# Optimization experiments

Measured on AMD Instinct MI355X. Metric: run time of the kernel, lower is better.

The kernel has to match this reference:

```python
import jax, jax.numpy as jnp
import numpy as np

DIM = 96
NUM_HEADS = 3
WIN = (4, 4, 4)
SHIFT = (2, 2, 2)
MLP_HID = 4 * DIM
EPS = 1e-5


def layer_norm(x, w, b):
    mu = jnp.mean(x, axis=-1, keepdims=True)
    var = jnp.var(x, axis=-1, keepdims=True)
    return (x - mu) * jax.lax.rsqrt(var + EPS) * w + b


def window_partition(x, ws):
    b, d, h, w, c = x.shape
    x = x.reshape(b, d // ws[0], ws[0], h // ws[1], ws[1], w // ws[2], ws[2], c)
    x = jnp.transpose(x, (0, 1, 3, 5, 2, 4, 6, 7))
    return x.reshape(-1, ws[0] * ws[1] * ws[2], c)


def window_reverse(windows, ws, dims):
    b, d, h, w = dims
    x = windows.reshape(b, d // ws[0], h // ws[1], w // ws[2], ws[0], ws[1], ws[2], -1)
    x = jnp.transpose(x, (0, 1, 4, 2, 5, 3, 6, 7))
    return x.reshape(b, d, h, w, -1)


def setup_inputs() -> dict:
    key = jax.random.key(0)
    ks = jax.random.split(key, 14)
    C, H3 = DIM, MLP_HID
    s = lambda k, shp, sc: (jax.random.normal(k, shp, dtype=jnp.float32) * sc)
    return {
        "x": jax.random.normal(ks[0], (2, 32, 64, 64, C), dtype=jnp.float32),
        "ln1_w": jnp.ones((C,), jnp.float32),
        "ln1_b": jnp.zeros((C,), jnp.float32),
        "qkv_w": s(ks[1], (3 * C, C), 0.02),
        "qkv_b": jnp.zeros((3 * C,), jnp.float32),
        "proj_w": s(ks[2], (C, C), 0.02),
        "proj_b": jnp.zeros((C,), jnp.float32),
        "ln2_w": jnp.ones((C,), jnp.float32),
        "ln2_b": jnp.zeros((C,), jnp.float32),
        "fc1_w": s(ks[3], (H3, C), 0.02),
        "fc1_b": jnp.zeros((H3,), jnp.float32),
        "fc2_w": s(ks[4], (C, H3), 0.02),
        "fc2_b": jnp.zeros((C,), jnp.float32),
    }


def reference(x, ln1_w, ln1_b, qkv_w, qkv_b, proj_w, proj_b, ln2_w, ln2_b,
              fc1_w, fc1_b, fc2_w, fc2_b):
    B, D, H, W, C = x.shape
    nh = NUM_HEADS
    hd = C // nh
    scale = hd ** -0.5
    N = WIN[0] * WIN[1] * WIN[2]

    shortcut = x
    h = layer_norm(x, ln1_w, ln1_b)
    # cyclic shift
    h = jnp.roll(h, shift=(-SHIFT[0], -SHIFT[1], -SHIFT[2]), axis=(1, 2, 3))
    xw = window_partition(h, WIN)                     # [B*nW, N, C]
    Bw = xw.shape[0]

    # window attention (no mask / no relative bias in original forward)
    qkv = xw @ qkv_w.T + qkv_b                        # [Bw, N, 3C]
    qkv = qkv.reshape(Bw, N, 3, nh, hd).transpose(2, 0, 3, 1, 4)
    q, k, v = qkv[0], qkv[1], qkv[2]                  # [Bw, nh, N, hd]
    attn = jnp.einsum('bhnd,bhmd->bhnm', q * scale, k)
    attn = jax.nn.softmax(attn, axis=-1)
    out = jnp.einsum('bhnm,bhmd->bhnd', attn, v)
    out = out.transpose(0, 2, 1, 3).reshape(Bw, N, C)
    out = out @ proj_w.T + proj_b

    h = window_reverse(out, WIN, (B, D, H, W))
    h = jnp.roll(h, shift=SHIFT, axis=(1, 2, 3))
    x = shortcut + h

    # MLP with exact GELU (torch nn.GELU default)
    m = layer_norm(x, ln2_w, ln2_b)
    m = jax.nn.gelu(m @ fc1_w.T + fc1_b, approximate=False)
    m = m @ fc2_w.T + fc2_b
    return x + m
```

## Files before the change

kernel.cpp:

```cpp
#include <hip/hip_runtime.h>
#include <hip/hip_bf16.h>
#include <math.h>

typedef __hip_bfloat16 bf16;
using short8 = __attribute__((ext_vector_type(8))) short;
using f32x4  = __attribute__((ext_vector_type(4))) float;

__device__ __forceinline__ bf16 f2b(float v){ return __float2bfloat16(v); }
__device__ __forceinline__ float gelu_exact(float v){ return 0.5f * v * (1.f + erff(v * 0.70710678118654752f)); }

__global__ __launch_bounds__(256)
void prep_weights(const float* __restrict__ qkv_w, const float* __restrict__ proj_w,
                  const float* __restrict__ fc1_w, const float* __restrict__ fc2_w,
                  bf16* __restrict__ ws)
{
    const int t = blockIdx.x * 256 + threadIdx.x;
    const int f = t >> 6;
    const int lane = t & 63;
    const float* W; int KT, fr; bf16* dst;
    if (f < 54)       { W = qkv_w;  KT = 3;  fr = f;       dst = ws; }
    else if (f < 72)  { W = proj_w; KT = 3;  fr = f - 54;  dst = ws + 54*512; }
    else if (f < 144) { W = fc1_w;  KT = 3;  fr = f - 72;  dst = ws + 72*512; }
    else              { W = fc2_w;  KT = 12; fr = f - 144; dst = ws + 144*512; }
    const int nt = fr / KT, kt = fr % KT;
    const int Kin = KT * 32;
    const float* src = W + (nt*16 + (lane & 15))*Kin + kt*32 + 8*(lane >> 4);
    bf16* d = dst + fr*512 + lane*8;
    #pragma unroll
    for (int i = 0; i < 8; i++) d[i] = f2b(src[i]);
}

__global__ __launch_bounds__(256, 3)
void swin_fused(const float* __restrict__ x,
                const float* __restrict__ ln1_w, const float* __restrict__ ln1_b,
                const float* __restrict__ qkv_b, const float* __restrict__ proj_b,
                const float* __restrict__ ln2_w, const float* __restrict__ ln2_b,
                const float* __restrict__ fc1_b, const float* __restrict__ fc2_b,
                const bf16* __restrict__ wsf,
                float* __restrict__ out)
{
    __shared__ int tok_off[64];
    __shared__ __align__(16) char pool[50688];
    bf16 (*ln_s)[104] = (bf16(*)[104])(pool + 0);
    bf16 (*q_s)[40]   = (bf16(*)[40])(pool + 13312);
    bf16 (*k_s)[40]   = (bf16(*)[40])(pool + 18432);
    bf16 (*vt_s)[72]  = (bf16(*)[72])(pool + 23552);
    bf16 (*p_s)[72]   = (bf16(*)[72])(pool + 28160);
    bf16 (*ao_s)[104] = (bf16(*)[104])(pool + 37376);
    bf16 (*ln2s)[104] = ao_s;
    bf16 (*hid)[392]  = (bf16(*)[392])(pool + 0);

    const int tid = threadIdx.x;
    const int win = blockIdx.x;
    const int b  = win >> 11;
    const int wd = (win >> 8) & 7;
    const int wh = (win >> 4) & 15;
    const int ww = win & 15;

    if (tid < 64) {
        const int n  = tid;
        const int df = (wd*4 + (n >> 4)       + 2) & 31;
        const int hf = (wh*4 + ((n >> 2) & 3) + 2) & 63;
        const int wf = (ww*4 + (n & 3)        + 2) & 63;
        tok_off[n] = (((b*32 + df)*64 + hf)*64 + wf) * 96;
    }
    __syncthreads();

    {
        const int lane = tid & 63;
        const int n    = (tid >> 6)*16 + (lane >> 2);
        const int sub  = lane & 3;
        const float4* xr4 = (const float4*)(x + tok_off[n] + sub*24);
        float4 va[6];
        float s = 0.f, ss = 0.f;
        #pragma unroll
        for (int i = 0; i < 6; i++) {
            va[i] = xr4[i];
            s  += va[i].x + va[i].y + va[i].z + va[i].w;
            ss += va[i].x*va[i].x + va[i].y*va[i].y + va[i].z*va[i].z + va[i].w*va[i].w;
        }
        s += __shfl_xor(s, 1); ss += __shfl_xor(ss, 1);
        s += __shfl_xor(s, 2); ss += __shfl_xor(ss, 2);
        const float mean = s * (1.f/96.f);
        const float var  = ss * (1.f/96.f) - mean*mean;
        const float inv  = rsqrtf(var + 1e-5f);
        #pragma unroll
        for (int i = 0; i < 6; i++) {
            const float vv[4] = {va[i].x, va[i].y, va[i].z, va[i].w};
            #pragma unroll
            for (int j2 = 0; j2 < 4; j2++) {
                const int c = sub*24 + i*4 + j2;
                ln_s[n][c] = f2b((vv[j2] - mean) * inv * ln1_w[c] + ln1_b[c]);
            }
        }
    }
    __syncthreads();

    const int w    = tid >> 6;
    const int lane = tid & 63;
    const int lc   = lane & 15;
    const int lr   = lane >> 4;
    const int m0   = w * 16;
    const int tokr = m0 + lr*4;
    const float scale = 0.17677669529663688f;

    short8 lnA[3];
    #pragma unroll
    for (int kt = 0; kt < 3; kt++)
        lnA[kt] = *(const short8*)&ln_s[m0 + lc][kt*32 + 8*lr];

    for (int h = 0; h < 3; h++) {
        #pragma unroll
        for (int nt2 = 0; nt2 < 2; nt2++) {
            const int dd = nt2*16 + lc;
            {
                f32x4 acc = {0.f,0.f,0.f,0.f};
                #pragma unroll
                for (int kt = 0; kt < 3; kt++)
                    acc = __builtin_amdgcn_mfma_f32_16x16x32_bf16(
                        lnA[kt], *(const short8*)(wsf + ((2*h+nt2)*3+kt)*512 + lane*8), acc, 0,0,0);
                const float bias = qkv_b[h*32 + dd];
                #pragma unroll
                for (int r = 0; r < 4; r++)
                    q_s[tokr + r][dd] = f2b((acc[r] + bias) * scale);
            }
            {
                f32x4 acc = {0.f,0.f,0.f,0.f};
                #pragma unroll
                for (int kt = 0; kt < 3; kt++)
                    acc = __builtin_amdgcn_mfma_f32_16x16x32_bf16(
                        lnA[kt], *(const short8*)(wsf + ((6+2*h+nt2)*3+kt)*512 + lane*8), acc, 0,0,0);
                const float bias = qkv_b[96 + h*32 + dd];
                #pragma unroll
                for (int r = 0; r < 4; r++)
                    k_s[tokr + r][dd] = f2b(acc[r] + bias);
            }
            {
                f32x4 acc = {0.f,0.f,0.f,0.f};
                #pragma unroll
                for (int kt = 0; kt < 3; kt++)
                    acc = __builtin_amdgcn_mfma_f32_16x16x32_bf16(
                        *(const short8*)(wsf + ((12+2*h+nt2)*3+kt)*512 + lane*8), lnA[kt], acc, 0,0,0);
                #pragma unroll
                for (int r = 0; r < 4; r++) {
                    const int dl = nt2*16 + lr*4 + r;
                    vt_s[dl][m0 + lc] = f2b(acc[r] + qkv_b[192 + h*32 + dl]);
                }
            }
        }
        __syncthreads();

        {
            const short8 qf = *(const short8*)&q_s[m0 + lc][8*lr];
            f32x4 sacc[4];
            #pragma unroll
            for (int nt = 0; nt < 4; nt++) {
                f32x4 z = {0.f,0.f,0.f,0.f};
                sacc[nt] = __builtin_amdgcn_mfma_f32_16x16x32_bf16(
                    qf, *(const short8*)&k_s[nt*16 + lc][8*lr], z, 0,0,0);
            }
            #pragma unroll
            for (int r = 0; r < 4; r++) {
                float mx = fmaxf(fmaxf(sacc[0][r], sacc[1][r]), fmaxf(sacc[2][r], sacc[3][r]));
                mx = fmaxf(mx, __shfl_xor(mx, 1));
                mx = fmaxf(mx, __shfl_xor(mx, 2));
                mx = fmaxf(mx, __shfl_xor(mx, 4));
                mx = fmaxf(mx, __shfl_xor(mx, 8));
                float e[4], sum = 0.f;
                #pragma unroll
                for (int nt = 0; nt < 4; nt++) { e[nt] = __expf(sacc[nt][r] - mx); sum += e[nt]; }
                sum += __shfl_xor(sum, 1);
                sum += __shfl_xor(sum, 2);
                sum += __shfl_xor(sum, 4);
                sum += __shfl_xor(sum, 8);
                const float rs = 1.f / sum;
                #pragma unroll
                for (int nt = 0; nt < 4; nt++)
                    p_s[tokr + r][nt*16 + lc] = f2b(e[nt] * rs);
            }
        }

        {
            short8 pf[2];
            #pragma unroll
            for (int kt = 0; kt < 2; kt++)
                pf[kt] = *(const short8*)&p_s[m0 + lc][kt*32 + 8*lr];
            #pragma unroll
            for (int nt = 0; nt < 2; nt++) {
                f32x4 acc = {0.f,0.f,0.f,0.f};
                #pragma unroll
                for (int kt = 0; kt < 2; kt++)
                    acc = __builtin_amdgcn_mfma_f32_16x16x32_bf16(
                        pf[kt], *(const short8*)&vt_s[nt*16 + lc][kt*32 + 8*lr], acc, 0,0,0);
                #pragma unroll
                for (int r = 0; r < 4; r++)
                    ao_s[tokr + r][h*32 + nt*16 + lc] = f2b(acc[r]);
            }
        }
        __syncthreads();
    }

    f32x4 xv[6];
    {
        short8 af[3];
        #pragma unroll
        for (int kt = 0; kt < 3; kt++)
            af[kt] = *(const short8*)&ao_s[m0 + lc][kt*32 + 8*lr];
        const bf16* pw = wsf + 54*512;
        #pragma unroll
        for (int nt = 0; nt < 6; nt++) {
            f32x4 acc = {0.f,0.f,0.f,0.f};
            #pragma unroll
            for (int kt = 0; kt < 3; kt++)
                acc = __builtin_amdgcn_mfma_f32_16x16x32_bf16(
                    af[kt], *(const short8*)(pw + (nt*3+kt)*512 + lane*8), acc, 0,0,0);
            const int c = nt*16 + lc;
            const float bias = proj_b[c];
            #pragma unroll
            for (int r = 0; r < 4; r++)
                xv[nt][r] = x[tok_off[tokr + r] + c] + acc[r] + bias;
        }
    }

    {
        float wl[6], bl[6];
        #pragma unroll
        for (int nt = 0; nt < 6; nt++) { wl[nt] = ln2_w[nt*16 + lc]; bl[nt] = ln2_b[nt*16 + lc]; }
        #pragma unroll
        for (int r = 0; r < 4; r++) {
            float s = 0.f, ss = 0.f;
            #pragma unroll
            for (int nt = 0; nt < 6; nt++) { const float v = xv[nt][r]; s += v; ss += v*v; }
            s += __shfl_xor(s, 1); ss += __shfl_xor(ss, 1);
            s += __shfl_xor(s, 2); ss += __shfl_xor(ss, 2);
            s += __shfl_xor(s, 4); ss += __shfl_xor(ss, 4);
            s += __shfl_xor(s, 8); ss += __shfl_xor(ss, 8);
            const float mean = s * (1.f/96.f);
            const float var  = ss * (1.f/96.f) - mean*mean;
            const float inv  = rsqrtf(var + 1e-5f);
            #pragma unroll
            for (int nt = 0; nt < 6; nt++)
                ln2s[tokr + r][nt*16 + lc] = f2b((xv[nt][r] - mean) * inv * wl[nt] + bl[nt]);
        }
    }

    short8 afr[3];
    #pragma unroll
    for (int kt = 0; kt < 3; kt++)
        afr[kt] = *(const short8*)&ln2s[m0 + lc][kt*32 + 8*lr];
    __syncthreads();

    {
        const bf16* w1f = wsf + 72*512;
        #pragma unroll
        for (int nt = 0; nt < 24; nt += 2) {
            short8 b0[3], b1[3];
            #pragma unroll
            for (int kt = 0; kt < 3; kt++) {
                b0[kt] = *(const short8*)(w1f + ((nt  )*3 + kt)*512 + lane*8);
                b1[kt] = *(const short8*)(w1f + ((nt+1)*3 + kt)*512 + lane*8);
            }
            f32x4 a0 = {0.f,0.f,0.f,0.f}, a1 = {0.f,0.f,0.f,0.f};
            #pragma unroll
            for (int kt = 0; kt < 3; kt++) {
                a0 = __builtin_amdgcn_mfma_f32_16x16x32_bf16(afr[kt], b0[kt], a0, 0,0,0);
                a1 = __builtin_amdgcn_mfma_f32_16x16x32_bf16(afr[kt], b1[kt], a1, 0,0,0);
            }
            const int j0 = nt*16 + lc;
            const float bi0 = fc1_b[j0], bi1 = fc1_b[j0 + 16];
            #pragma unroll
            for (int r = 0; r < 4; r++) {
                hid[tokr + r][j0]      = f2b(gelu_exact(a0[r] + bi0));
                hid[tokr + r][j0 + 16] = f2b(gelu_exact(a1[r] + bi1));
            }
        }
    }

    {
        short8 af2[12];
        #pragma unroll
        for (int kt = 0; kt < 12; kt++)
            af2[kt] = *(const short8*)&hid[m0 + lc][kt*32 + 8*lr];
        const bf16* w2f = wsf + 144*512;
        #pragma unroll
        for (int nt = 0; nt < 6; nt++) {
            f32x4 acc = {0.f,0.f,0.f,0.f};
            #pragma unroll
            for (int kt = 0; kt < 12; kt++)
                acc = __builtin_amdgcn_mfma_f32_16x16x32_bf16(
                    af2[kt], *(const short8*)(w2f + (nt*12 + kt)*512 + lane*8), acc, 0,0,0);
            const int c = nt*16 + lc;
            const float bias = fc2_b[c];
            #pragma unroll
            for (int r = 0; r < 4; r++)
                out[tok_off[tokr + r] + c] = xv[nt][r] + acc[r] + bias;
        }
    }
}

extern "C" void kernel_launch(void* const* d_in, const int* in_sizes, int n_in,
                              void* d_out, int out_size, void* d_ws, size_t ws_size,
                              hipStream_t stream)
{
    const float* x      = (const float*)d_in[0];
    const float* ln1_w  = (const float*)d_in[1];
    const float* ln1_b  = (const float*)d_in[2];
    const float* qkv_w  = (const float*)d_in[3];
    const float* qkv_b  = (const float*)d_in[4];
    const float* proj_w = (const float*)d_in[5];
    const float* proj_b = (const float*)d_in[6];
    const float* ln2_w  = (const float*)d_in[7];
    const float* ln2_b  = (const float*)d_in[8];
    const float* fc1_w  = (const float*)d_in[9];
    const float* fc1_b  = (const float*)d_in[10];
    const float* fc2_w  = (const float*)d_in[11];
    const float* fc2_b  = (const float*)d_in[12];
    float* out = (float*)d_out;
    bf16* wsf  = (bf16*)d_ws;

    prep_weights<<<54, 256, 0, stream>>>(qkv_w, proj_w, fc1_w, fc2_w, wsf);
    swin_fused<<<4096, 256, 0, stream>>>(x, ln1_w, ln1_b, qkv_b, proj_b,
                                         ln2_w, ln2_b, fc1_b, fc2_b, wsf, out);
}
```

Measured before the change: 341.7 us.

## Cut LDS footprint via register LayerNorm and chunked MLP hidden buffer

LN1 is now computed straight into MFMA A-fragments in registers, so the ln_s shared buffer goes away. Token offsets are recomputed per thread rather than kept in shared memory. The fc1→fc2 hidden activation is processed in two 192-wide chunks, which halves the hidden LDS buffer. Together these shrink shared memory enough to raise launch bounds to 4 blocks per CU. The costs are more __syncthreads inside the MLP loop, extra register pressure under the tighter bound (possible spills), and duplicated x loads. The weight-prep kernel also gets vectorized loads and stores.

After: 372.4 us. 1.09x slower.

```diff
diff --git a/kernel.cpp b/kernel.cpp
--- a/kernel.cpp
+++ b/kernel.cpp
@@ -25,12 +25,15 @@
     const int nt = fr / KT, kt = fr % KT;
     const int Kin = KT * 32;
     const float* src = W + (nt*16 + (lane & 15))*Kin + kt*32 + 8*(lane >> 4);
-    bf16* d = dst + fr*512 + lane*8;
-    #pragma unroll
-    for (int i = 0; i < 8; i++) d[i] = f2b(src[i]);
+    const float4 s0 = *(const float4*)src;
+    const float4 s1 = *(const float4*)(src + 4);
+    union { bf16 h[8]; short8 v; } u;
+    u.h[0]=f2b(s0.x); u.h[1]=f2b(s0.y); u.h[2]=f2b(s0.z); u.h[3]=f2b(s0.w);
+    u.h[4]=f2b(s1.x); u.h[5]=f2b(s1.y); u.h[6]=f2b(s1.z); u.h[7]=f2b(s1.w);
+    *(short8*)(dst + fr*512 + lane*8) = u.v;
 }
 
-__global__ __launch_bounds__(256, 3)
+__global__ __launch_bounds__(256, 4)
 void swin_fused(const float* __restrict__ x,
                 const float* __restrict__ ln1_w, const float* __restrict__ ln1_b,
                 const float* __restrict__ qkv_b, const float* __restrict__ proj_b,
@@ -39,16 +42,14 @@
                 const bf16* __restrict__ wsf,
                 float* __restrict__ out)
 {
-    __shared__ int tok_off[64];
-    __shared__ __align__(16) char pool[50688];
-    bf16 (*ln_s)[104] = (bf16(*)[104])(pool + 0);
-    bf16 (*q_s)[40]   = (bf16(*)[40])(pool + 13312);
-    bf16 (*k_s)[40]   = (bf16(*)[40])(pool + 18432);
-    bf16 (*vt_s)[72]  = (bf16(*)[72])(pool + 23552);
-    bf16 (*p_s)[72]   = (bf16(*)[72])(pool + 28160);
-    bf16 (*ao_s)[104] = (bf16(*)[104])(pool + 37376);
+    __shared__ __align__(16) char pool[37376];
+    bf16 (*q_s)[40]   = (bf16(*)[40])(pool + 0);
+    bf16 (*k_s)[40]   = (bf16(*)[40])(pool + 5120);
+    bf16 (*vt_s)[72]  = (bf16(*)[72])(pool + 10240);
+    bf16 (*p_s)[72]   = (bf16(*)[72])(pool + 14848);
+    bf16 (*ao_s)[104] = (bf16(*)[104])(pool + 24064);
     bf16 (*ln2s)[104] = ao_s;
-    bf16 (*hid)[392]  = (bf16(*)[392])(pool + 0);
+    bf16 (*hid)[200]  = (bf16(*)[200])(pool + 0);
 
     const int tid = threadIdx.x;
     const int win = blockIdx.x;
@@ -56,45 +57,6 @@
     const int wd = (win >> 8) & 7;
     const int wh = (win >> 4) & 15;
     const int ww = win & 15;
-
-    if (tid < 64) {
-        const int n  = tid;
-        const int df = (wd*4 + (n >> 4)       + 2) & 31;
-        const int hf = (wh*4 + ((n >> 2) & 3) + 2) & 63;
-        const int wf = (ww*4 + (n & 3)        + 2) & 63;
-        tok_off[n] = (((b*32 + df)*64 + hf)*64 + wf) * 96;
-    }
-    __syncthreads();
-
-    {
-        const int lane = tid & 63;
-        const int n    = (tid >> 6)*16 + (lane >> 2);
-        const int sub  = lane & 3;
-        const float4* xr4 = (const float4*)(x + tok_off[n] + sub*24);
-        float4 va[6];
-        float s = 0.f, ss = 0.f;
-        #pragma unroll
-        for (int i = 0; i < 6; i++) {
-            va[i] = xr4[i];
-            s  += va[i].x + va[i].y + va[i].z + va[i].w;
-            ss += va[i].x*va[i].x + va[i].y*va[i].y + va[i].z*va[i].z + va[i].w*va[i].w;
-        }
-        s += __shfl_xor(s, 1); ss += __shfl_xor(ss, 1);
-        s += __shfl_xor(s, 2); ss += __shfl_xor(ss, 2);
-        const float mean = s * (1.f/96.f);
-        const float var  = ss * (1.f/96.f) - mean*mean;
-        const float inv  = rsqrtf(var + 1e-5f);
-        #pragma unroll
-        for (int i = 0; i < 6; i++) {
-            const float vv[4] = {va[i].x, va[i].y, va[i].z, va[i].w};
-            #pragma unroll
-            for (int j2 = 0; j2 < 4; j2++) {
-                const int c = sub*24 + i*4 + j2;
-                ln_s[n][c] = f2b((vv[j2] - mean) * inv * ln1_w[c] + ln1_b[c]);
-            }
-        }
-    }
-    __syncthreads();
 
     const int w    = tid >> 6;
     const int lane = tid & 63;
@@ -104,10 +66,50 @@
     const int tokr = m0 + lr*4;
     const float scale = 0.17677669529663688f;
 
+    auto tok_offset = [&](int n) -> int {
+        const int df = (wd*4 + (n >> 4)       + 2) & 31;
+        const int hf = (wh*4 + ((n >> 2) & 3) + 2) & 63;
+        const int wf = (ww*4 + (n & 3)        + 2) & 63;
+        return (((b*32 + df)*64 + hf)*64 + wf) * 96;
+    };
+    const int myTok = tok_offset(m0 + lc);
+    int toks[4];
+    #pragma unroll
+    for (int r = 0; r < 4; r++) toks[r] = tok_offset(tokr + r);
+
     short8 lnA[3];
-    #pragma unroll
-    for (int kt = 0; kt < 3; kt++)
-        lnA[kt] = *(const short8*)&ln_s[m0 + lc][kt*32 + 8*lr];
+    {
+        float v[3][8];
+        float s = 0.f, ss = 0.f;
+        #pragma unroll
+        for (int kt = 0; kt < 3; kt++) {
+            const float4 a = *(const float4*)(x + myTok + kt*32 + 8*lr);
+            const float4 c = *(const float4*)(x + myTok + kt*32 + 8*lr + 4);
+            v[kt][0]=a.x; v[kt][1]=a.y; v[kt][2]=a.z; v[kt][3]=a.w;
+            v[kt][4]=c.x; v[kt][5]=c.y; v[kt][6]=c.z; v[kt][7]=c.w;
+            #pragma unroll
+            for (int i = 0; i < 8; i++) { s += v[kt][i]; ss += v[kt][i]*v[kt][i]; }
+        }
+        s += __shfl_xor(s, 16); ss += __shfl_xor(ss, 16);
+        s += __shfl_xor(s, 32); ss += __shfl_xor(ss, 32);
+        const float mean = s * (1.f/96.f);
+        const float var  = ss * (1.f/96.f) - mean*mean;
+        const float inv  = rsqrtf(var + 1e-5f);
+        #pragma unroll
+        for (int kt = 0; kt < 3; kt++) {
+            const float4 w0 = *(const float4*)(ln1_w + kt*32 + 8*lr);
+            const float4 w1 = *(const float4*)(ln1_w + kt*32 + 8*lr + 4);
+            const float4 b0 = *(const float4*)(ln1_b + kt*32 + 8*lr);
+            const float4 b1 = *(const float4*)(ln1_b + kt*32 + 8*lr + 4);
+            const float wv[8] = {w0.x,w0.y,w0.z,w0.w,w1.x,w1.y,w1.z,w1.w};
+            const float bv[8] = {b0.x,b0.y,b0.z,b0.w,b1.x,b1.y,b1.z,b1.w};
+            union { bf16 h[8]; short8 v8; } u;
+            #pragma unroll
+            for (int i = 0; i < 8; i++)
+                u.h[i] = f2b((v[kt][i] - mean) * inv * wv[i] + bv[i]);
+            lnA[kt] = u.v8;
+        }
+    }
 
     for (int h = 0; h < 3; h++) {
         #pragma unroll
@@ -218,7 +220,7 @@
             const float bias = proj_b[c];
             #pragma unroll
             for (int r = 0; r < 4; r++)
-                xv[nt][r] = x[tok_off[tokr + r] + c] + acc[r] + bias;
+                xv[nt][r] = x[toks[r] + c] + acc[r] + bias;
         }
     }
 
@@ -250,51 +252,62 @@
         afr[kt] = *(const short8*)&ln2s[m0 + lc][kt*32 + 8*lr];
     __syncthreads();
 
-    {
-        const bf16* w1f = wsf + 72*512;
-        #pragma unroll
-        for (int nt = 0; nt < 24; nt += 2) {
-            short8 b0[3], b1[3];
+    const bf16* w1f = wsf + 72*512;
+    const bf16* w2f = wsf + 144*512;
+    f32x4 acc2[6];
+    #pragma unroll
+    for (int nt = 0; nt < 6; nt++) acc2[nt] = (f32x4){0.f,0.f,0.f,0.f};
+
+    #pragma unroll
+    for (int c = 0; c < 2; c++) {
+        #pragma unroll
+        for (int g = 0; g < 6; g++) {
+            short8 bfB[2][3];
+            #pragma unroll
+            for (int q = 0; q < 2; q++) {
+                const int nt = c*12 + g*2 + q;
+                #pragma unroll
+                for (int kt = 0; kt < 3; kt++)
+                    bfB[q][kt] = *(const short8*)(w1f + (nt*3 + kt)*512 + lane*8);
+            }
+            f32x4 a0 = {0.f,0.f,0.f,0.f}, a1 = {0.f,0.f,0.f,0.f};
             #pragma unroll
             for (int kt = 0; kt < 3; kt++) {
-                b0[kt] = *(const short8*)(w1f + ((nt  )*3 + kt)*512 + lane*8);
-                b1[kt] = *(const short8*)(w1f + ((nt+1)*3 + kt)*512 + lane*8);
-            }
-            f32x4 a0 = {0.f,0.f,0.f,0.f}, a1 = {0.f,0.f,0.f,0.f};
-            #pragma unroll
-            for (int kt = 0; kt < 3; kt++) {
-                a0 = __builtin_amdgcn_mfma_f32_16x16x32_bf16(afr[kt], b0[kt], a0, 0,0,0);
-                a1 = __builtin_amdgcn_mfma_f32_16x16x32_bf16(afr[kt], b1[kt], a1, 0,0,0);
-            }
-            const int j0 = nt*16 + lc;
+                a0 = __builtin_amdgcn_mfma_f32_16x16x32_bf16(afr[kt], bfB[0][kt], a0, 0,0,0);
+                a1 = __builtin_amdgcn_mfma_f32_16x16x32_bf16(afr[kt], bfB[1][kt], a1, 0,0,0);
+            }
+            const int ntl = g*2;
+            const int j0  = (c*12 + ntl)*16 + lc;
             const float bi0 = fc1_b[j0], bi1 = fc1_b[j0 + 16];
             #pragma unroll
             for (int r = 0; r < 4; r++) {
-                hid[tokr + r][j0]      = f2b(gelu_exact(a0[r] + bi0));
-                hid[tokr + r][j0 + 16] = f2b(gelu_exact(a1[r] + bi1));
-            }
-        }
-    }
-
-    {
-        short8 af2[12];
-        #pragma unroll
-        for (int kt = 0; kt < 12; kt++)
+                hid[tokr + r][ntl*16 + lc]      = f2b(gelu_exact(a0[r] + bi0));
+                hid[tokr + r][(ntl+1)*16 + lc]  = f2b(gelu_exact(a1[r] + bi1));
+            }
+            __syncthreads();
+        }
+
+        short8 af2[6];
+        #pragma unroll
+        for (int kt = 0; kt < 6; kt++)
             af2[kt] = *(const short8*)&hid[m0 + lc][kt*32 + 8*lr];
-        const bf16* w2f = wsf + 144*512;
         #pragma unroll
         for (int nt = 0; nt < 6; nt++) {
-            f32x4 acc = {0.f,0.f,0.f,0.f};
-            #pragma unroll
-            for (int kt = 0; kt < 12; kt++)
-                acc = __builtin_amdgcn_mfma_f32_16x16x32_bf16(
-                    af2[kt], *(const short8*)(w2f + (nt*12 + kt)*512 + lane*8), acc, 0,0,0);
-            const int c = nt*16 + lc;
-            const float bias = fc2_b[c];
-            #pragma unroll
-            for (int r = 0; r < 4; r++)
-                out[tok_off[tokr + r] + c] = xv[nt][r] + acc[r] + bias;
-        }
+            #pragma unroll
+            for (int kt = 0; kt < 6; kt++)
+                acc2[nt] = __builtin_amdgcn_mfma_f32_16x16x32_bf16(
+                    af2[kt], *(const short8*)(w2f + (nt*12 + c*6 + kt)*512 + lane*8), acc2[nt], 0,0,0);
+        }
+        __syncthreads();
+    }
+
+    #pragma unroll
+    for (int nt = 0; nt < 6; nt++) {
+        const int c = nt*16 + lc;
+        const float bias = fc2_b[c];
+        #pragma unroll
+        for (int r = 0; r < 4; r++)
+            out[toks[r] + c] = xv[nt][r] + acc2[nt][r] + bias;
     }
 }
 
```
